# Performance work log

Hardware: AMD Instinct MI355X
Metric: run time of the kernel (lower is better)

## Reference

```python
import jax, jax.numpy as jnp
import numpy as np
from jax import lax

EPS = 1e-7
MAX_NORM = 1.0 - 1e-5

# ---- Poincare ball (c=1) primitives ----

def _norm(x):
    return jnp.sqrt(jnp.sum(x * x, -1, keepdims=True) + EPS)

def proj(x):
    n = _norm(x)
    return x * jnp.minimum(1.0, MAX_NORM / n)

def expmap0(v):
    n = _norm(v)
    return jnp.tanh(n) * v / n

def logmap0(x):
    n = _norm(x)
    return jnp.arctanh(jnp.clip(n, 0.0, MAX_NORM)) * x / n

def mobius_add(u, v):
    uv = jnp.sum(u * v, -1, keepdims=True)
    uu = jnp.sum(u * u, -1, keepdims=True)
    vv = jnp.sum(v * v, -1, keepdims=True)
    num = (1.0 + 2.0 * uv + vv) * u + (1.0 - uu) * v
    den = 1.0 + 2.0 * uv + uu * vv
    return num / den

# Mobius matvec M (x) x = expmap0(logmap0(x) @ M^T)

def gru_step(h, x, Wr, Wz, Wh, Ur, Uz, Uh, br, bz, bh):
    lh = logmap0(h)
    lx = logmap0(x)
    r = jax.nn.sigmoid(logmap0(mobius_add(mobius_add(expmap0(lh @ Wr.T), expmap0(lx @ Ur.T)), br)))
    z = jax.nn.sigmoid(logmap0(mobius_add(mobius_add(expmap0(lh @ Wz.T), expmap0(lx @ Uz.T)), bz)))
    htil = mobius_add(mobius_add(expmap0((r * lh) @ Wh.T), expmap0(lx @ Uh.T)), bh)
    delta = mobius_add(-h, htil)
    return proj(mobius_add(h, expmap0(z * logmap0(delta))))


def hyperplane_logits(X, P, A):
    # Hyperbolic MLR (Ganea et al.) without materializing [N,V,d]:
    # (-p)(+)x = (-alpha*p + beta*x) / gamma
    xx = jnp.sum(X * X, -1)                  # [N]
    pp = jnp.sum(P * P, -1)                  # [V]
    aa = jnp.sqrt(jnp.sum(A * A, -1) + EPS)  # [V]
    pa = jnp.sum(P * A, -1)                  # [V]
    px = X @ P.T                             # [N,V]
    xa = X @ A.T                             # [N,V]
    alpha = 1.0 - 2.0 * px + xx[:, None]
    beta = (1.0 - pp)[None, :]
    gamma = 1.0 - 2.0 * px + pp[None, :] * xx[:, None]
    da = (-alpha * pa[None, :] + beta * xa) / gamma
    dd = (alpha * alpha * pp[None, :] - 2.0 * alpha * beta * px + beta * beta * xx[:, None]) / (gamma * gamma)
    lam = 2.0 / (1.0 - pp)                   # conformal factor at p_k
    arg = 2.0 * da / ((1.0 - dd) * aa[None, :] + EPS)
    return (lam * aa)[None, :] * jnp.arcsinh(arg)


VOCAB, EMB, HID, LAYERS = 10000, 512, 512, 3
B, S = 16, 128


def setup_inputs() -> dict:
    key = jax.random.key(0)
    ks = jax.random.split(key, 16)
    inp = jax.random.randint(ks[0], (B, S), 0, VOCAB)
    tgt = jax.random.randint(ks[1], (B, S), 0, VOCAB)
    E = proj(0.01 * jax.random.normal(ks[2], (VOCAB, EMB), jnp.float32))
    E = E.at[0].set(0.0)  # padding_idx=0
    mk = lambda k: 0.05 * jax.random.normal(k, (LAYERS, HID, HID), jnp.float32)
    Wr, Wz, Wh = mk(ks[3]), mk(ks[4]), mk(ks[5])
    Ur, Uz, Uh = mk(ks[6]), mk(ks[7]), mk(ks[8])
    mb = lambda k: proj(0.01 * jax.random.normal(k, (LAYERS, HID), jnp.float32))
    br, bz, bh = mb(ks[9]), mb(ks[10]), mb(ks[11])
    P = proj(0.01 * jax.random.normal(ks[12], (VOCAB, HID), jnp.float32))
    A = 0.05 * jax.random.normal(ks[13], (VOCAB, HID), jnp.float32)
    return {"input": inp, "target": tgt, "E": E, "Wr": Wr, "Wz": Wz, "Wh": Wh,
            "Ur": Ur, "Uz": Uz, "Uh": Uh, "br": br, "bz": bz, "bh": bh, "P": P, "A": A}


def reference(input, target, E, Wr, Wz, Wh, Ur, Uz, Uh, br, bz, bh, P, A):
    b, s = input.shape
    x = E[input]                       # [B,S,H] points on the ball
    x = jnp.transpose(x, (1, 0, 2))    # [S,B,H]
    for l in range(LAYERS):
        params = (Wr[l], Wz[l], Wh[l], Ur[l], Uz[l], Uh[l],
                  br[l][None, :], bz[l][None, :], bh[l][None, :])
        def step(h, xt, params=params):
            h = gru_step(h, xt, *params)
            return h, h
        h0 = jnp.zeros((b, HID), x.dtype)
        _, x = lax.scan(step, h0, x)   # [S,B,H]
    X = x.transpose(1, 0, 2).reshape(-1, HID)          # [B*S,H]
    logits = hyperplane_logits(X, P, A)                # [B*S,V]
    logp = jax.nn.log_softmax(logits, axis=-1)
    nll = -jnp.take_along_axis(logp, target.reshape(-1, 1), axis=1)[:, 0]
    return jnp.mean(nll).reshape(1)
```

## Files before the change

### kernel.cpp

```cpp
#include <hip/hip_runtime.h>
#include <hip/hip_bf16.h>
#include <math.h>

#define EPSF 1e-7f
#define MAXNRM 0.99999f

static constexpr int Bb = 16, Ss = 128, Hh = 512, Vv = 10000, Ll = 3;
static constexpr int Nn = Bb * Ss;
static constexpr int VT = 625;

typedef __attribute__((ext_vector_type(4))) float f32x4;
typedef __attribute__((ext_vector_type(8))) short short8v;
typedef _Float16 h2 __attribute__((ext_vector_type(2)));

__device__ inline float4 ld4(const float* p){ return *(const float4*)p; }
__device__ inline void st4(float* p, float4 v){ *(float4*)p = v; }
__device__ inline float dot4(float4 a, float4 b){ return a.x*b.x + a.y*b.y + a.z*b.z + a.w*b.w; }
__device__ inline float sigm(float x){ return 1.f/(1.f + expf(-x)); }
__device__ inline unsigned short f2bf(float f){
  __hip_bfloat16 h = __float2bfloat16(f);
  return __builtin_bit_cast(unsigned short, h);
}
__device__ inline unsigned short f2h(float f){
  _Float16 h = (_Float16)f;
  return __builtin_bit_cast(unsigned short, h);
}
__device__ inline float rsum64f(float v){
  v+=__shfl_xor(v,32); v+=__shfl_xor(v,16); v+=__shfl_xor(v,8);
  v+=__shfl_xor(v,4);  v+=__shfl_xor(v,2);  v+=__shfl_xor(v,1); return v;
}
__device__ inline float dot4_e5m2(uint u, h2 L0, h2 L1, float acc){
  uint p01 = __builtin_amdgcn_perm(u, 0u, 0x05000400u);
  uint p23 = __builtin_amdgcn_perm(u, 0u, 0x07000600u);
  acc = __builtin_amdgcn_fdot2(__builtin_bit_cast(h2,p01), L0, acc, false);
  acc = __builtin_amdgcn_fdot2(__builtin_bit_cast(h2,p23), L1, acc, false);
  return acc;
}
__device__ inline void stg_scu(uint* p, uint v){
  asm volatile("global_store_dword %0, %1, off sc0 sc1" :: "v"(p), "v"(v) : "memory");
}
__device__ inline uint ldg_scu(const uint* p){
  uint r;
  asm volatile("global_load_dword %0, %1, off sc0 sc1\n\ts_waitcnt vmcnt(0)"
               : "=v"(r) : "v"(p) : "memory");
  return r;
}

template<int NR>
__device__ __forceinline__ void stream_e5m2_rows(const uint* __restrict__ W8m,
    const uint* src2, float (*part)[Hh], int row0, int lane, int prow){
  const int j8 = lane*8;
  const uint* W = W8m + (size_t)row0*Hh + j8;
  float acc[8] = {0,0,0,0,0,0,0,0};
  #pragma unroll 4
  for(int i=0;i<NR;i++){
    uint4 wa = *(const uint4*)(W + (size_t)i*Hh);
    uint4 wb = *(const uint4*)(W + (size_t)i*Hh + 4);
    uint2 L = *(const uint2*)&src2[(row0+i)*2];
    h2 L0=__builtin_bit_cast(h2,L.x), L1=__builtin_bit_cast(h2,L.y);
    acc[0]=dot4_e5m2(wa.x,L0,L1,acc[0]); acc[1]=dot4_e5m2(wa.y,L0,L1,acc[1]);
    acc[2]=dot4_e5m2(wa.z,L0,L1,acc[2]); acc[3]=dot4_e5m2(wa.w,L0,L1,acc[3]);
    acc[4]=dot4_e5m2(wb.x,L0,L1,acc[4]); acc[5]=dot4_e5m2(wb.y,L0,L1,acc[5]);
    acc[6]=dot4_e5m2(wb.z,L0,L1,acc[6]); acc[7]=dot4_e5m2(wb.w,L0,L1,acc[7]);
  }
  float* d = &part[prow][j8];
  *(f32x4*)d = (f32x4){acc[0],acc[1],acc[2],acc[3]};
  *(f32x4*)(d+4) = (f32x4){acc[4],acc[5],acc[6],acc[7]};
}
__device__ __forceinline__ void stream_e5m2_pair(const uint* __restrict__ WA,
    const uint* __restrict__ WB, const uint* src2, float (*part)[Hh], int tid, int j8){
  int hf = tid >> 9;
  int kq = (tid >> 6) & 7;
  const uint* W = (hf ? WB : WA) + (size_t)(kq*16)*Hh + j8;
  float acc[8] = {0,0,0,0,0,0,0,0};
  #pragma unroll 4
  for(int i=0;i<16;i++){
    uint4 wa = *(const uint4*)(W + (size_t)i*Hh);
    uint4 wb = *(const uint4*)(W + (size_t)i*Hh + 4);
    uint2 L = *(const uint2*)&src2[(kq*16+i)*2];
    h2 L0=__builtin_bit_cast(h2,L.x), L1=__builtin_bit_cast(h2,L.y);
    acc[0]=dot4_e5m2(wa.x,L0,L1,acc[0]); acc[1]=dot4_e5m2(wa.y,L0,L1,acc[1]);
    acc[2]=dot4_e5m2(wa.z,L0,L1,acc[2]); acc[3]=dot4_e5m2(wa.w,L0,L1,acc[3]);
    acc[4]=dot4_e5m2(wb.x,L0,L1,acc[4]); acc[5]=dot4_e5m2(wb.y,L0,L1,acc[5]);
    acc[6]=dot4_e5m2(wb.z,L0,L1,acc[6]); acc[7]=dot4_e5m2(wb.w,L0,L1,acc[7]);
  }
  float* d = &part[hf*8+kq][j8];
  *(f32x4*)d = (f32x4){acc[0],acc[1],acc[2],acc[3]};
  *(f32x4*)(d+4) = (f32x4){acc[4],acc[5],acc[6],acc[7]};
}

__global__ __launch_bounds__(256) void k_packW8(const float* __restrict__ Wr,
    const float* __restrict__ Wz, uint* __restrict__ W8){
  int jt = blockIdx.x, kt = blockIdx.y, lm = blockIdx.z;
  int l = lm>>1, m = lm&1;
  const float* src = (m==0?Wr:Wz) + (size_t)l*Hh*Hh;
  uint* dst = W8 + (size_t)lm*(128*Hh);
  __shared__ float t[64][65];
  int tid = threadIdx.x;
  #pragma unroll
  for(int p=0;p<4;p++){
    int row = p*16 + (tid>>4);
    int c4 = (tid&15)*4;
    st4(&t[row][c4], ld4(src + ((size_t)(jt*64+row))*Hh + kt*64 + c4));
  }
  __syncthreads();
  #pragma unroll
  for(int p=0;p<4;p++){
    int k4l = p*4 + (tid>>6);
    int j_l = tid & 63;
    uint u = 0;
    #pragma unroll
    for(int i=0;i<4;i++){
      ushort b16 = __builtin_bit_cast(ushort, (_Float16)t[j_l][k4l*4+i]);
      uint b8 = (uint)((ushort)(b16 + 0x80) >> 8);
      u |= b8 << (8*i);
    }
    dst[(size_t)(kt*16 + k4l)*Hh + jt*64 + j_l] = u;
  }
}
__global__ __launch_bounds__(256) void k_packW8s(const float* __restrict__ W, uint* __restrict__ W8){
  int jt = blockIdx.x, kt = blockIdx.y, l = blockIdx.z;
  const float* src = W + (size_t)l*Hh*Hh;
  uint* dst = W8 + (size_t)l*(128*Hh);
  __shared__ float t[64][65];
  int tid = threadIdx.x;
  #pragma unroll
  for(int p=0;p<4;p++){
    int row = p*16 + (tid>>4);
    int c4 = (tid&15)*4;
    st4(&t[row][c4], ld4(src + ((size_t)(jt*64+row))*Hh + kt*64 + c4));
  }
  __syncthreads();
  #pragma unroll
  for(int p=0;p<4;p++){
    int k4l = p*4 + (tid>>6);
    int j_l = tid & 63;
    uint u = 0;
    #pragma unroll
    for(int i=0;i<4;i++){
      ushort b16 = __builtin_bit_cast(ushort, (_Float16)t[j_l][k4l*4+i]);
      uint b8 = (uint)((ushort)(b16 + 0x80) >> 8);
      u |= b8 << (8*i);
    }
    dst[(size_t)(kt*16 + k4l)*Hh + jt*64 + j_l] = u;
  }
}

__global__ void k_predots(const float* __restrict__ XR, const float* __restrict__ XZ,
                          const float* __restrict__ XH,
                          const float* __restrict__ br, const float* __restrict__ bz,
                          const float* __restrict__ bh, float* __restrict__ pubX){
  int n = blockIdx.x; int tid = threadIdx.x;
  float s0=0,s1=0,s2=0,s3=0,s4=0,s5=0;
  for(int i=tid;i<Hh;i+=128){
    float xr=XR[(size_t)n*Hh+i], xz=XZ[(size_t)n*Hh+i], xh=XH[(size_t)n*Hh+i];
    s0+=xr*xr; s1+=xr*br[i]; s2+=xz*xz; s3+=xz*bz[i]; s4+=xh*xh; s5+=xh*bh[i];
  }
  __shared__ float red[2][6];
  s0=rsum64f(s0); s1=rsum64f(s1); s2=rsum64f(s2);
  s3=rsum64f(s3); s4=rsum64f(s4); s5=rsum64f(s5);
  int w = tid>>6;
  if((tid&63)==0){ red[w][0]=s0; red[w][1]=s1; red[w][2]=s2; red[w][3]=s3; red[w][4]=s4; red[w][5]=s5; }
  __syncthreads();
  if(tid==0){
    #pragma unroll
    for(int d=0;d<6;d++) pubX[(size_t)n*6+d] = red[0][d]+red[1][d];
  }
}

__global__ void k_pav(const float* __restrict__ P, const float* __restrict__ A,
                      float* __restrict__ pp, float* __restrict__ aa, float* __restrict__ pa){
  int w = threadIdx.x >> 6, lane = threadIdx.x & 63;
  int v = blockIdx.x*4 + w;
  const float4* Pr = (const float4*)(P + (size_t)v*Hh);
  const float4* Ar = (const float4*)(A + (size_t)v*Hh);
  float sp=0, sa=0, spa=0;
  #pragma unroll
  for(int i=0;i<2;i++){
    int k4 = lane*2 + i;
    float4 pv = Pr[k4], av = Ar[k4];
    sp += dot4(pv,pv); sa += dot4(av,av); spa += dot4(pv,av);
  }
  for(int o=32;o;o>>=1){ sp+=__shfl_down(sp,o); sa+=__shfl_down(sa,o); spa+=__shfl_down(spa,o); }
  if(lane==0){ pp[v]=sp; aa[v]=sqrtf(sa+EPSF); pa[v]=spa; }
}

__global__ void k_embed(const int* __restrict__ inp, const float* __restrict__ E, float* __restrict__ X){
  int n = blockIdx.x; int t = n >> 4, b = n & 15;
  int tok = inp[b*Ss + t];
  int i = threadIdx.x;
  st4(X + (size_t)n*Hh + i*4, ld4(E + (size_t)tok*Hh + i*4));
}

__global__ void k_logmap(const float* __restrict__ X, float* __restrict__ LX){
  int n = blockIdx.x; int t = threadIdx.x;
  __shared__ float sred[2];
  float4 v = ld4(X + (size_t)n*Hh + t*4);
  float ss = dot4(v,v);
  for(int o=32;o;o>>=1) ss += __shfl_down(ss,o);
  if((t&63)==0) sred[t>>6] = ss;
  __syncthreads();
  ss = sred[0]+sred[1];
  float nn = sqrtf(ss + EPSF);
  float sc = atanhf(fminf(nn, MAXNRM)) / nn;
  v.x*=sc; v.y*=sc; v.z*=sc; v.w*=sc;
  st4(LX + (size_t)n*Hh + t*4, v);
}

__global__ void k_expmap(float* __restrict__ XR, float* __restrict__ XZ, float* __restrict__ XH){
  float* Xp = blockIdx.y==0 ? XR : (blockIdx.y==1 ? XZ : XH);
  int n = blockIdx.x; int t = threadIdx.x;
  __shared__ float sred[2];
  float4 v = ld4(Xp + (size_t)n*Hh + t*4);
  float ss = dot4(v,v);
  for(int o=32;o;o>>=1) ss += __shfl_down(ss,o);
  if((t&63)==0) sred[t>>6] = ss;
  __syncthreads();
  ss = sred[0]+sred[1];
  float nn = sqrtf(ss + EPSF);
  float sc = tanhf(nn) / nn;
  v.x*=sc; v.y*=sc; v.z*=sc; v.w*=sc;
  st4(Xp + (size_t)n*Hh + t*4, v);
}

__global__ __launch_bounds__(256) void k_gemm(const float* __restrict__ A4,
    const float* __restrict__ U0, const float* __restrict__ U1, const float* __restrict__ U2,
    float* __restrict__ O0, float* __restrict__ O1, float* __restrict__ O2){
  __shared__ float As[16][65], Bs[16][65];
  int jb = blockIdx.x;
  int nb = blockIdx.y;
  int mat = jb >> 3; int j0 = (jb & 7)*64;
  const float* Bm = mat==0?U0 : (mat==1?U1:U2);
  float* Om       = mat==0?O0 : (mat==1?O1:O2);
  int tid = threadIdx.x;
  int lr = tid >> 2, lq = tid & 3;
  int tx = tid & 15, ty = tid >> 4;
  float acc[4][4] = {};
  for(int kb=0; kb<Hh; kb+=16){
    float4 av = ld4(A4 + (size_t)(nb*64+lr)*Hh + kb + lq*4);
    float4 bv = ld4(Bm + (size_t)(j0+lr)*Hh + kb + lq*4);
    As[lq*4+0][lr]=av.x; As[lq*4+1][lr]=av.y; As[lq*4+2][lr]=av.z; As[lq*4+3][lr]=av.w;
    Bs[lq*4+0][lr]=bv.x; Bs[lq*4+1][lr]=bv.y; Bs[lq*4+2][lr]=bv.z; Bs[lq*4+3][lr]=bv.w;
    __syncthreads();
    #pragma unroll
    for(int kk=0;kk<16;kk++){
      float a0=As[kk][ty*4+0], a1=As[kk][ty*4+1], a2=As[kk][ty*4+2], a3=As[kk][ty*4+3];
      float b0=Bs[kk][tx*4+0], b1=Bs[kk][tx*4+1], b2=Bs[kk][tx*4+2], b3=Bs[kk][tx*4+3];
      acc[0][0]+=a0*b0; acc[0][1]+=a0*b1; acc[0][2]+=a0*b2; acc[0][3]+=a0*b3;
      acc[1][0]+=a1*b0; acc[1][1]+=a1*b1; acc[1][2]+=a1*b2; acc[1][3]+=a1*b3;
      acc[2][0]+=a2*b0; acc[2][1]+=a2*b1; acc[2][2]+=a2*b2; acc[2][3]+=a2*b3;
      acc[3][0]+=a3*b0; acc[3][1]+=a3*b1; acc[3][2]+=a3*b2; acc[3][3]+=a3*b3;
    }
    __syncthreads();
  }
  for(int i=0;i<4;i++)
    for(int j2=0;j2<4;j2++)
      Om[(size_t)(nb*64+ty*4+i)*Hh + j0 + tx*4 + j2] = acc[i][j2];
}

__global__ __launch_bounds__(1024) void k_mega(
    const float* __restrict__ XR, const float* __restrict__ XZ, const float* __restrict__ XH,
    const float* __restrict__ pubX,
    const uint* __restrict__ W8, const uint* __restrict__ W8h,
    const uint* __restrict__ U8, const uint* __restrict__ U8h,
    const float* __restrict__ brA, const float* __restrict__ bzA, const float* __restrict__ bhA,
    uint* __restrict__ LH0, uint* __restrict__ LH1,
    int* __restrict__ flags0, int* __restrict__ flags1,
    float* __restrict__ Xfin){
  const int xcd = blockIdx.x & 7;
  const int layer = xcd >> 1;
  if(layer >= 3) return;
  const int b = (xcd & 1)*8 + (blockIdx.x >> 3);
  const int tid = threadIdx.x;
  const int lane = tid & 63, wv = tid >> 6;
  const int j8 = lane * 8;

  const uint* W8r = W8 + (size_t)(layer*2+0)*128*Hh;
  const uint* W8z = W8 + (size_t)(layer*2+1)*128*Hh;
  const uint* Wh8 = W8h + (size_t)layer*128*Hh;
  const uint* U8r = U8 + (size_t)(layer*2+0)*128*Hh;
  const uint* U8z = U8 + (size_t)(layer*2+1)*128*Hh;
  const uint* Uh8 = U8h + (size_t)layer*128*Hh;
  const float* br = brA + layer*Hh;
  const float* bz = bzA + layer*Hh;
  const float* bh = bhA + layer*Hh;
  uint* outLH = (layer==0)? LH0 : (layer==1)? LH1 : nullptr;
  int* outF = (layer==0)? flags0 : (layer==1)? flags1 : nullptr;
  const uint* inLH = (layer==1)? LH0 : LH1;
  int* inF = (layer==1)? flags0 : flags1;

  __shared__ float part[16][Hh];
  __shared__ float mr_s[Hh], mz_s[Hh], mur_s[Hh], muz_s[Hh];
  __shared__ uint  lh2_s[256], ap2_s[256], lx2_s[256];
  __shared__ float bias0[Hh], bias1[Hh], bias2[Hh];
  __shared__ float partA[8][16];
  __shared__ float partB[8][18];
  __shared__ float coefA_s[12], coefB_s[8], bb_s[4];

  if(tid<256) lh2_s[tid]=0u;
  for(int i=tid;i<Hh;i+=1024){ bias0[i]=br[i]; bias1[i]=bz[i]; bias2[i]=bh[i]; }
  __syncthreads();
  {
    float p0=0,p1=0,p2=0;
    if(tid<Hh){ float a=bias0[tid],b2=bias1[tid],c2=bias2[tid]; p0=a*a; p1=b2*b2; p2=c2*c2; }
    p0=rsum64f(p0); p1=rsum64f(p1); p2=rsum64f(p2);
    if(tid<Hh && lane==0){ partB[wv][0]=p0; partB[wv][1]=p1; partB[wv][2]=p2; }
    __syncthreads();
    if(tid==0){
      float a=0,b2=0,c2=0;
      for(int i=0;i<8;i++){ a+=partB[i][0]; b2+=partB[i][1]; c2+=partB[i][2]; }
      bb_s[0]=a; bb_s[1]=b2; bb_s[2]=c2;
    }
    __syncthreads();
  }

  float h = 0.f;
  float Sh = 0.f, hxh = 0.f, hbh = 0.f;

  for(int ts=0; ts<Ss; ts++){
    const size_t row = (size_t)(ts*Bb + b)*Hh;
    const size_t lrow = (size_t)(ts*Bb + b)*256;

    if(layer == 0){
      float xr=0,xz=0,xh=0;
      if(tid<512){ xr=XR[row+tid]; xz=XZ[row+tid]; xh=XH[row+tid]; }
      stream_e5m2_pair(W8r, W8z, lh2_s, part, tid, j8);
      __syncthreads();
      float mr=0.f, mz=0.f;
      if(tid<512){
        float s0=0, s1=0;
        #pragma unroll
        for(int q=0;q<8;q++){ s0+=part[q][tid]; s1+=part[8+q][tid]; }
        mr=s0; mz=s1; mr_s[tid]=s0;
        float brc=bias0[tid], bzc=bias1[tid], bhc=bias2[tid];
        float p0=mr*mr, p1=mr*xr, p2=mr*brc, p3=mz*mz, p4=mz*xz, p5=mz*bzc, p6=h*xh, p7=h*bhc;
        p0=rsum64f(p0); p1=rsum64f(p1); p2=rsum64f(p2); p3=rsum64f(p3);
        p4=rsum64f(p4); p5=rsum64f(p5); p6=rsum64f(p6); p7=rsum64f(p7);
        if(lane==0){
          partA[wv][0]=p0; partA[wv][1]=p1; partA[wv][2]=p2; partA[wv][3]=p3;
          partA[wv][4]=p4; partA[wv][5]=p5; partA[wv][6]=p6; partA[wv][7]=p7;
        }
      }
      __syncthreads();
      if(tid==0){
        float s[8];
        #pragma unroll
        for(int d=0;d<8;d++){
          float x=0;
          for(int i=0;i<8;i++) x+=partA[i][d];
          s[d]=x;
        }
        hxh=s[6]; hbh=s[7];
        const float* px = pubX + (size_t)(ts*Bb+b)*6;
        float xrxr=px[0], xrbr=px[1], xzxz=px[2], xzbz=px[3];
        float bbr=bb_s[0], bbz=bb_s[1];
        float nm=sqrtf(s[0]+EPSF), se=tanhf(nm)/nm;
        float uv=se*s[1], uu=se*se*s[0];
        float den=1.f+2.f*uv+uu*xrxr;
        float a1=(1.f+2.f*uv+xrxr)*se/den, a2=(1.f-uu)/den;
        float uv2=a1*s[2]+a2*xrbr;
        float uu2=a1*a1*s[0]+2.f*a1*a2*s[1]+a2*a2*xrxr;
        float den2=1.f+2.f*uv2+uu2*bbr;
        float b1=(1.f+2.f*uv2+bbr)/den2, b2c=(1.f-uu2)/den2;
        float c1=b1*a1, c2=b1*a2, c3=b2c;
        float n2sq=c1*c1*s[0]+c2*c2*xrxr+c3*c3*bbr+2.f*(c1*c2*s[1]+c1*c3*s[2]+c2*c3*xrbr);
        float nn2=sqrtf(n2sq+EPSF);
        float s_r=atanhf(fminf(nn2,MAXNRM))/nn2;
        coefA_s[0]=s_r*c1; coefA_s[1]=s_r*c2; coefA_s[2]=s_r*c3;
        float nmz=sqrtf(s[3]+EPSF), sez=tanhf(nmz)/nmz;
        float uvz=sez*s[4], uuz=sez*sez*s[3];
        float denz=1.f+2.f*uvz+uuz*xzxz;
        float az1=(1.f+2.f*uvz+xzxz)*sez/denz, az2=(1.f-uuz)/denz;
        float uvz2=az1*s[5]+az2*xzbz;
        float uuz2=az1*az1*s[3]+2.f*az1*az2*s[4]+az2*az2*xzxz;
        float denz2=1.f+2.f*uvz2+uuz2*bbz;
        float bz1=(1.f+2.f*uvz2+bbz)/denz2, bz2=(1.f-uuz2)/denz2;
        float cz1=bz1*az1, cz2=bz1*az2, cz3=bz2;
        float nz2sq=cz1*cz1*s[3]+cz2*cz2*xzxz+cz3*cz3*bbz+2.f*(cz1*cz2*s[4]+cz1*cz3*s[5]+cz2*cz3*xzbz);
        float nnz2=sqrtf(nz2sq+EPSF);
        float s_z=atanhf(fminf(nnz2,MAXNRM))/nnz2;
        coefA_s[3]=s_z*cz1; coefA_s[4]=s_z*cz2; coefA_s[5]=s_z*cz3;
        coefA_s[6]=px[4]; coefA_s[7]=px[4]; coefA_s[8]=px[5];
      }
      __syncthreads();
      if(tid<256){
        int e0 = tid*2;
        float ca=coefA_s[0], cb=coefA_s[1], cc2=coefA_s[2];
        h2 lp = __builtin_bit_cast(h2, lh2_s[tid]);
        float r0 = sigm(ca*mr_s[e0]   + cb*XR[row+e0]   + cc2*bias0[e0]);
        float r1 = sigm(ca*mr_s[e0+1] + cb*XR[row+e0+1] + cc2*bias0[e0+1]);
        ap2_s[tid] = (uint)f2h(r0*(float)lp[0]) | ((uint)f2h(r1*(float)lp[1])<<16);
      }
      __syncthreads();
      stream_e5m2_rows<8>(Wh8, ap2_s, part, (tid>>6)*8, lane, tid>>6);
      __syncthreads();
      float mh=0.f, z=0.f;
      if(tid<512){
        float s=0;
        #pragma unroll
        for(int q=0;q<16;q++) s+=part[q][tid];
        mh=s;
        float bhc=bias2[tid], bzc=bias1[tid];
        z = sigm(coefA_s[3]*mz + coefA_s[4]*xz + coefA_s[5]*bzc);
        float eh=z*h, em=z*mh, ex=z*xh, eb=z*bhc;
        float p[18] = {mh*mh, mh*xh, mh*bhc, h*mh,
                       eh*eh, eh*em, eh*ex, eh*eb,
                       em*em, em*ex, em*eb, ex*ex, ex*eb, eb*eb,
                       h*eh, h*em, h*ex, h*eb};
        #pragma unroll
        for(int d=0;d<18;d++) p[d]=rsum64f(p[d]);
        if(lane==0){
          #pragma unroll
          for(int d=0;d<18;d++) partB[wv][d]=p[d];
        }
      }
      __syncthreads();
      if(tid==0){
        float dsum[18];
        #pragma unroll
        for(int d=0;d<18;d++){
          float x=0;
          for(int i=0;i<8;i++) x+=partB[i][d];
          dsum[d]=x;
        }
        float d0=dsum[0], d1=dsum[1], d2=dsum[2], d3=dsum[3];
        float Ghh=dsum[4], Ghm=dsum[5], Ghx=dsum[6], Ghb=dsum[7];
        float Gmm=dsum[8], Gmx=dsum[9], Gmb=dsum[10];
        float Gxx=dsum[11], Gxb=dsum[12], Gbb=dsum[13];
        float Heh=dsum[14], Hem=dsum[15], Hex=dsum[16], Heb=dsum[17];
        float xhxh=coefA_s[7], xhbh=coefA_s[8];
        float bbh=bb_s[2]; float Shb=Sh;
        float nm3=sqrtf(d0+EPSF), se3=tanhf(nm3)/nm3;
        float uvh=se3*d1, uuh=se3*se3*d0;
        float denh=1.f+2.f*uvh+uuh*xhxh;
        float a1p=(1.f+2.f*uvh+xhxh)*se3/denh, a2p=(1.f-uuh)/denh;
        float uv2h=a1p*d2+a2p*xhbh;
        float uu2h=a1p*a1p*d0+2.f*a1p*a2p*d1+a2p*a2p*xhxh;
        float den2h=1.f+2.f*uv2h+uu2h*bbh;
        float b1p=(1.f+2.f*uv2h+bbh)/den2h, b2p=(1.f-uu2h)/den2h;
        float c1p=b1p*a1p, c2p=b1p*a2p, c3p=b2p;
        float h_htil=c1p*d3+c2p*hxh+c3p*hbh;
        float htil2=c1p*c1p*d0+c2p*c2p*xhxh+c3p*c3p*bbh
                  +2.f*(c1p*c2p*d1+c1p*c3p*d2+c2p*c3p*xhbh);
        float denD=1.f-2.f*h_htil+Shb*htil2;
        float dd1=(1.f-2.f*h_htil+htil2)/denD, dd2=(1.f-Shb)/denD;
        float g0=-dd1, g1=dd2*c1p, g2=dd2*c2p, g3=dd2*c3p;
        float del2=g0*g0*Shb+g1*g1*d0+g2*g2*xhxh+g3*g3*bbh
                 +2.f*(g0*g1*d3+g0*g2*hxh+g0*g3*hbh+g1*g2*d1+g1*g3*d2+g2*g3*xhbh);
        float ndl=sqrtf(del2+EPSF);
        float sld=atanhf(fminf(ndl,MAXNRM))/ndl;
        float Qe=g0*g0*Ghh+g1*g1*Gmm+g2*g2*Gxx+g3*g3*Gbb
               +2.f*(g0*g1*Ghm+g0*g2*Ghx+g0*g3*Ghb+g1*g2*Gmx+g1*g3*Gmb+g2*g3*Gxb);
        float Le=g0*Heh+g1*Hem+g2*Hex+g3*Heb;
        float Sww=sld*sld*Qe;
        float Shw=sld*Le;
        float nw=sqrtf(Sww+EPSF), sew=tanhf(nw)/nw;
        float uvw=sew*Shw, vvw=sew*sew*Sww;
        float denw=1.f+2.f*uvw+Shb*vvw;
        float q1=(1.f+2.f*uvw+vvw)/denw, q2=((1.f-Shb)/denw)*sew;
        float n2h=q1*q1*Shb+2.f*q1*q2*Shw+q2*q2*Sww;
        float nrm=sqrtf(n2h+EPSF);
        float scl=fminf(1.f, MAXNRM/nrm);
        float Shn=scl*scl*n2h;
        float nh2=sqrtf(Shn+EPSF);
        float slh=atanhf(fminf(nh2,MAXNRM))/nh2;
        coefB_s[0]=scl*q1; coefB_s[1]=scl*q2*sld;
        coefB_s[2]=g0; coefB_s[3]=g1; coefB_s[4]=g2; coefB_s[5]=g3;
        coefB_s[6]=slh;
        Sh=Shn;
      }
      __syncthreads();
      if(tid<512){
        float qc1=coefB_s[0], qc2=coefB_s[1];
        float g0=coefB_s[2], g1=coefB_s[3], g2=coefB_s[4], g3=coefB_s[5];
        float slh=coefB_s[6];
        float dl = g0*h + g1*mh + g2*xh + g3*bias2[tid];
        float hn = qc1*h + qc2*z*dl;
        h = hn;
        float lh = slh*hn;
        float lhp = __shfl_xor(lh, 1);
        if(!(tid&1)){
          uint pk = (uint)f2h(lh) | ((uint)f2h(lhp)<<16);
          lh2_s[tid>>1] = pk;
          stg_scu(outLH + lrow + (tid>>1), pk);
        }
      }
      __syncthreads();
      if(tid==0) __hip_atomic_store(outF + b*Ss + ts, 1, __ATOMIC_RELAXED, __HIP_MEMORY_SCOPE_AGENT);
    } else {
      if(tid < 512){
        if(wv < 4) stream_e5m2_rows<32>(W8r, lh2_s, part, wv*32, lane, wv);
        else       stream_e5m2_rows<32>(W8z, lh2_s, part, (wv-4)*32, lane, wv);
      } else if(tid < 768){
        int idx = tid - 512;
        while(__hip_atomic_load(inF + b*Ss + ts, __ATOMIC_RELAXED, __HIP_MEMORY_SCOPE_AGENT) == 0)
          __builtin_amdgcn_s_sleep(1);
        lx2_s[idx] = ldg_scu(inLH + lrow + idx);
      }
      __syncthreads();

      float mr=0.f, mz=0.f;
      if(tid < 512){
        mr = part[0][tid]+part[1][tid]+part[2][tid]+part[3][tid];
        mz = part[4][tid]+part[5][tid]+part[6][tid]+part[7][tid];
        mr_s[tid]=mr; mz_s[tid]=mz;
        float p0=mr*mr, p1=mr*bias0[tid], p2=mz*mz, p3=mz*bias1[tid];
        p0=rsum64f(p0); p1=rsum64f(p1); p2=rsum64f(p2); p3=rsum64f(p3);
        if(lane==0){ partA[wv][0]=p0; partA[wv][1]=p1; partA[wv][2]=p2; partA[wv][3]=p3; }
      } else {
        if(wv < 12) stream_e5m2_rows<32>(U8r, lx2_s, part, (wv-8)*32, lane, wv);
        else        stream_e5m2_rows<32>(U8z, lx2_s, part, (wv-12)*32, lane, wv);
      }
      __syncthreads();

      if(tid < 512){
        stream_e5m2_rows<16>(Uh8, lx2_s, part, wv*16, lane, wv);
      } else {
        int j = tid - 512;
        float mur = part[8][j]+part[9][j]+part[10][j]+part[11][j];
        float muz = part[12][j]+part[13][j]+part[14][j]+part[15][j];
        mur_s[j]=mur; muz_s[j]=muz;
        float p5=mur*mur, p6=mur*bias0[j], p7=muz*muz, p8=muz*bias1[j];
        float p9=mr_s[j]*mur, p10=mz_s[j]*muz;
        p5=rsum64f(p5); p6=rsum64f(p6); p7=rsum64f(p7);
        p8=rsum64f(p8); p9=rsum64f(p9); p10=rsum64f(p10);
        if(lane==0){
          partA[wv-8][5]=p5; partA[wv-8][6]=p6; partA[wv-8][7]=p7;
          partA[wv-8][8]=p8; partA[wv-8][9]=p9; partA[wv-8][10]=p10;
        }
      }
      __syncthreads();

      float muh=0.f;
      if(tid<512){
        float s=0;
        #pragma unroll
        for(int q=0;q<8;q++) s+=part[q][tid];
        muh=s;
        float bhc=bias2[tid];
        float p11=muh*muh, p12=h*muh, p13=muh*bhc, p14=h*bhc;
        p11=rsum64f(p11); p12=rsum64f(p12); p13=rsum64f(p13); p14=rsum64f(p14);
        if(lane==0){ partA[wv][11]=p11; partA[wv][12]=p12; partA[wv][13]=p13; partA[wv][14]=p14; }
      }
      __syncthreads();

      if(tid==0){
        float S[15];
        #pragma unroll
        for(int d=0;d<15;d++){
          float xS=0;
          for(int i=0;i<8;i++) xS+=partA[i][d];
          S[d]=xS;
        }
        float bbr=bb_s[0], bbz=bb_s[1];
        float nur=sqrtf(S[5]+EPSF), se_r=tanhf(nur)/nur;
        float nuz=sqrtf(S[7]+EPSF), se_z=tanhf(nuz)/nuz;
        float nuh=sqrtf(S[11]+EPSF), se_h=tanhf(nuh)/nuh;
        float s0=S[0], s1=se_r*S[9], s2=S[1];
        float xrxr=se_r*se_r*S[5], xrbr=se_r*S[6];
        float s3=S[2], s4=se_z*S[10], s5=S[3];
        float xzxz=se_z*se_z*S[7], xzbz=se_z*S[8];
        hxh = se_h*S[12]; hbh = S[14];
        float xhxh=se_h*se_h*S[11], xhbh=se_h*S[13];
        float nm=sqrtf(s0+EPSF), se=tanhf(nm)/nm;
        float uv=se*s1, uu=se*se*s0;
        float den=1.f+2.f*uv+uu*xrxr;
        float a1=(1.f+2.f*uv+xrxr)*se/den, a2=(1.f-uu)/den;
        float uv2=a1*s2+a2*xrbr;
        float uu2=a1*a1*s0+2.f*a1*a2*s1+a2*a2*xrxr;
        float den2=1.f+2.f*uv2+uu2*bbr;
        float b1=(1.f+2.f*uv2+bbr)/den2, b2c=(1.f-uu2)/den2;
        float c1=b1*a1, c2=b1*a2, c3=b2c;
        float n2sq=c1*c1*s0+c2*c2*xrxr+c3*c3*bbr+2.f*(c1*c2*s1+c1*c3*s2+c2*c3*xrbr);
        float nn2=sqrtf(n2sq+EPSF);
        float s_r=atanhf(fminf(nn2,MAXNRM))/nn2;
        coefA_s[0]=s_r*c1; coefA_s[1]=s_r*c2*se_r; coefA_s[2]=s_r*c3;
        float nmz=sqrtf(s3+EPSF), sez=tanhf(nmz)/nmz;
        float uvz=sez*s4, uuz=sez*sez*s3;
        float denz=1.f+2.f*uvz+uuz*xzxz;
        float az1=(1.f+2.f*uvz+xzxz)*sez/denz, az2=(1.f-uuz)/denz;
        float uvz2=az1*s5+az2*xzbz;
        float uuz2=az1*az1*s3+2.f*az1*az2*s4+az2*az2*xzxz;
        float denz2=1.f+2.f*uvz2+uuz2*bbz;
        float bz1=(1.f+2.f*uvz2+bbz)/denz2, bz2=(1.f-uuz2)/denz2;
        float cz1=bz1*az1, cz2=bz1*az2, cz3=bz2;
        float nz2sq=cz1*cz1*s3+cz2*cz2*xzxz+cz3*cz3*bbz+2.f*(cz1*cz2*s4+cz1*cz3*s5+cz2*cz3*xzbz);
        float nnz2=sqrtf(nz2sq+EPSF);
        float s_z=atanhf(fminf(nnz2,MAXNRM))/nnz2;
        coefA_s[3]=s_z*cz1; coefA_s[4]=s_z*cz2*se_z; coefA_s[5]=s_z*cz3;
        coefA_s[6]=se_h; coefA_s[7]=xhxh; coefA_s[8]=xhbh;
      }
      __syncthreads();

      if(tid<256){
        int e0 = tid*2;
        float ca=coefA_s[0], cbp=coefA_s[1], cc2=coefA_s[2];
        h2 lp = __builtin_bit_cast(h2, lh2_s[tid]);
        float r0 = sigm(ca*mr_s[e0]   + cbp*mur_s[e0]   + cc2*bias0[e0]);
        float r1 = sigm(ca*mr_s[e0+1] + cbp*mur_s[e0+1] + cc2*bias0[e0+1]);
        ap2_s[tid] = (uint)f2h(r0*(float)lp[0]) | ((uint)f2h(r1*(float)lp[1])<<16);
      }
      __syncthreads();

      stream_e5m2_rows<8>(Wh8, ap2_s, part, (tid>>6)*8, lane, tid>>6);
      __syncthreads();

      float mh=0.f, z=0.f;
      if(tid<512){
        float s=0;
        #pragma unroll
        for(int q=0;q<16;q++) s+=part[q][tid];
        mh=s;
        float se_h = coefA_s[6];
        float xh = se_h*muh;
        float bhc=bias2[tid], bzc=bias1[tid];
        z = sigm(coefA_s[3]*mz + coefA_s[4]*muz_s[tid] + coefA_s[5]*bzc);
        float eh=z*h, em=z*mh, ex=z*xh, eb=z*bhc;
        float p[18] = {mh*mh, mh*xh, mh*bhc, h*mh,
                       eh*eh, eh*em, eh*ex, eh*eb,
                       em*em, em*ex, em*eb, ex*ex, ex*eb, eb*eb,
                       h*eh, h*em, h*ex, h*eb};
        #pragma unroll
        for(int d=0;d<18;d++) p[d]=rsum64f(p[d]);
        if(lane==0){
          #pragma unroll
          for(int d=0;d<18;d++) partB[wv][d]=p[d];
        }
      }
      __syncthreads();

      if(tid==0){
        float dsum[18];
        #pragma unroll
        for(int d=0;d<18;d++){
          float xS=0;
          for(int i=0;i<8;i++) xS+=partB[i][d];
          dsum[d]=xS;
        }
        float d0=dsum[0], d1=dsum[1], d2=dsum[2], d3=dsum[3];
        float Ghh=dsum[4], Ghm=dsum[5], Ghx=dsum[6], Ghb=dsum[7];
        float Gmm=dsum[8], Gmx=dsum[9], Gmb=dsum[10];
        float Gxx=dsum[11], Gxb=dsum[12], Gbb=dsum[13];
        float Heh=dsum[14], Hem=dsum[15], Hex=dsum[16], Heb=dsum[17];
        float xhxh=coefA_s[7], xhbh=coefA_s[8];
        float bbh=bb_s[2]; float Shb=Sh;
        float nm3=sqrtf(d0+EPSF), se3=tanhf(nm3)/nm3;
        float uvh=se3*d1, uuh=se3*se3*d0;
        float denh=1.f+2.f*uvh+uuh*xhxh;
        float a1p=(1.f+2.f*uvh+xhxh)*se3/denh, a2p=(1.f-uuh)/denh;
        float uv2h=a1p*d2+a2p*xhbh;
        float uu2h=a1p*a1p*d0+2.f*a1p*a2p*d1+a2p*a2p*xhxh;
        float den2h=1.f+2.f*uv2h+uu2h*bbh;
        float b1p=(1.f+2.f*uv2h+bbh)/den2h, b2p=(1.f-uu2h)/den2h;
        float c1p=b1p*a1p, c2p=b1p*a2p, c3p=b2p;
        float h_htil=c1p*d3+c2p*hxh+c3p*hbh;
        float htil2=c1p*c1p*d0+c2p*c2p*xhxh+c3p*c3p*bbh
                  +2.f*(c1p*c2p*d1+c1p*c3p*d2+c2p*c3p*xhbh);
        float denD=1.f-2.f*h_htil+Shb*htil2;
        float dd1=(1.f-2.f*h_htil+htil2)/denD, dd2=(1.f-Shb)/denD;
        float g0=-dd1, g1=dd2*c1p, g2=dd2*c2p, g3=dd2*c3p;
        float del2=g0*g0*Shb+g1*g1*d0+g2*g2*xhxh+g3*g3*bbh
                 +2.f*(g0*g1*d3+g0*g2*hxh+g0*g3*hbh+g1*g2*d1+g1*g3*d2+g2*g3*xhbh);
        float ndl=sqrtf(del2+EPSF);
        float sld=atanhf(fminf(ndl,MAXNRM))/ndl;
        float Qe=g0*g0*Ghh+g1*g1*Gmm+g2*g2*Gxx+g3*g3*Gbb
               +2.f*(g0*g1*Ghm+g0*g2*Ghx+g0*g3*Ghb+g1*g2*Gmx+g1*g3*Gmb+g2*g3*Gxb);
        float Le=g0*Heh+g1*Hem+g2*Hex+g3*Heb;
        float Sww=sld*sld*Qe;
        float Shw=sld*Le;
        float nw=sqrtf(Sww+EPSF), sew=tanhf(nw)/nw;
        float uvw=sew*Shw, vvw=sew*sew*Sww;
        float denw=1.f+2.f*uvw+Shb*vvw;
        float q1=(1.f+2.f*uvw+vvw)/denw, q2=((1.f-Shb)/denw)*sew;
        float n2h=q1*q1*Shb+2.f*q1*q2*Shw+q2*q2*Sww;
        float nrm=sqrtf(n2h+EPSF);
        float scl=fminf(1.f, MAXNRM/nrm);
        float Shn=scl*scl*n2h;
        float nh2=sqrtf(Shn+EPSF);
        float slh=atanhf(fminf(nh2,MAXNRM))/nh2;
        coefB_s[0]=scl*q1; coefB_s[1]=scl*q2*sld;
        coefB_s[2]=g0; coefB_s[3]=g1; coefB_s[4]=g2; coefB_s[5]=g3;
        coefB_s[6]=slh;
        Sh=Shn;
      }
      __syncthreads();

      if(tid<512){
        float qc1=coefB_s[0], qc2=coefB_s[1];
        float g0=coefB_s[2], g1=coefB_s[3], g2=coefB_s[4], g3=coefB_s[5];
        float slh=coefB_s[6];
        float xh = coefA_s[6]*muh;
        float dl = g0*h + g1*mh + g2*xh + g3*bias2[tid];
        float hn = qc1*h + qc2*z*dl;
        h = hn;
        if(layer==2) Xfin[row + tid] = hn;
        float lh = slh*hn;
        float lhp = __shfl_xor(lh, 1);
        if(!(tid&1)){
          uint pk = (uint)f2h(lh) | ((uint)f2h(lhp)<<16);
          lh2_s[tid>>1] = pk;
          if(layer==1) stg_scu(outLH + lrow + (tid>>1), pk);
        }
      }
      __syncthreads();
      if(layer==1 && tid==0)
        __hip_atomic_store(outF + b*Ss + ts, 1, __ATOMIC_RELAXED, __HIP_MEMORY_SCOPE_AGENT);
    }
  }
}

__global__ __launch_bounds__(256) void k_packF(const float* __restrict__ src, ushort* __restrict__ dst){
  int vt = blockIdx.x;
  __shared__ float rows[16][516];
  int tid = threadIdx.x;
  #pragma unroll
  for(int p=0;p<8;p++){
    int idx = p*256 + tid;
    int row = idx >> 7, c4 = idx & 127;
    st4(&rows[row][c4*4], ld4(src + ((size_t)vt*16+row)*Hh + c4*4));
  }
  __syncthreads();
  #pragma unroll
  for(int p=0;p<4;p++){
    int idx = p*256 + tid;
    int kt = idx >> 6, lane = idx & 63;
    int vloc = lane & 15, k0 = kt*32 + ((lane>>4)&3)*8;
    union { ushort u[8]; uint4 v; } tt;
    #pragma unroll
    for(int i=0;i<8;i++) tt.u[i] = f2bf(rows[vloc][k0+i]);
    *(uint4*)(dst + (((size_t)vt*16 + kt)*64 + lane)*8) = tt.v;
  }
}

__global__ __launch_bounds__(256) void k_mlr2(
    const ushort* __restrict__ Xf, const ushort* __restrict__ Pf, const ushort* __restrict__ Af,
    const float* __restrict__ X, const float* __restrict__ pp, const float* __restrict__ aa,
    const float* __restrict__ pa, const int* __restrict__ tgt,
    float* __restrict__ pm, float* __restrict__ tl){
  int rb = blockIdx.x;
  int sp = blockIdx.y;
  int tid = threadIdx.x, lane = tid&63, w = tid>>6;
  __shared__ ushort Axf[4*16*64*8];
  __shared__ float xxp[64][4];
  __shared__ float xxs[64];
  #pragma unroll
  for(int p=0;p<16;p++){
    int idx = p*256 + tid;
    ((uint4*)Axf)[idx] = ((const uint4*)Xf)[(size_t)rb*4096 + idx];
  }
  {
    int row = tid>>2, seg = tid&3;
    const float* xr = X + ((size_t)rb*64 + row)*Hh + seg*128;
    float s=0;
    #pragma unroll
    for(int i=0;i<32;i++){ float4 v4 = ld4(xr+i*4); s += dot4(v4,v4); }
    xxp[row][seg]=s;
  }
  __syncthreads();
  if(tid<64) xxs[tid] = xxp[tid][0]+xxp[tid][1]+xxp[tid][2]+xxp[tid][3];
  __syncthreads();

  float mM[16], sS[16]; int tokv[16];
  #pragma unroll
  for(int rt=0;rt<4;rt++)
    #pragma unroll
    for(int i=0;i<4;i++){
      int idx=rt*4+i;
      int rr = rb*64 + rt*16 + (lane>>4)*4 + i;
      tokv[idx] = tgt[(rr&15)*Ss + (rr>>4)];
      mM[idx] = -3.0e38f; sS[idx]=0.f;
    }

  for(int vt = sp*4 + w; vt < VT; vt += 32){
    int v = vt*16 + (lane&15);
    float ppv = pp[v], aav = aa[v], pav = pa[v];
    f32x4 aP[4], aA[4];
    #pragma unroll
    for(int rt=0;rt<4;rt++){ aP[rt]=(f32x4){0,0,0,0}; aA[rt]=(f32x4){0,0,0,0}; }
    const short8v* Pb = (const short8v*)(Pf + (size_t)vt*8192);
    const short8v* Ab = (const short8v*)(Af + (size_t)vt*8192);
    #pragma unroll
    for(int kt=0;kt<16;kt++){
      short8v bP = Pb[kt*64+lane];
      short8v bA = Ab[kt*64+lane];
      #pragma unroll
      for(int rt=0;rt<4;rt++){
        short8v a = *(const short8v*)&Axf[(((size_t)rt*16+kt)*64+lane)*8];
        aP[rt] = __builtin_amdgcn_mfma_f32_16x16x32_bf16(a, bP, aP[rt], 0,0,0);
        aA[rt] = __builtin_amdgcn_mfma_f32_16x16x32_bf16(a, bA, aA[rt], 0,0,0);
      }
    }
    float be = 1.f - ppv;
    float lamaa = (2.f/be)*aav;
    #pragma unroll
    for(int rt=0;rt<4;rt++)
      #pragma unroll
      for(int i=0;i<4;i++){
        int idx = rt*4+i;
        int rl = rt*16 + (lane>>4)*4 + i;
        float px = aP[rt][i], xa = aA[rt][i];
        float xx = xxs[rl];
        float al = 1.f - 2.f*px + xx;
        float gm = 1.f - 2.f*px + ppv*xx;
        float da = (-al*pav + be*xa)/gm;
        float dd = (al*al*ppv - 2.f*al*be*px + be*be*xx)/(gm*gm);
        float arg = 2.f*da/((1.f-dd)*aav + EPSF);
        float lg = lamaa*asinhf(arg);
        if(v == tokv[idx]) tl[rb*64 + rl] = lg;
        if(lg > mM[idx]){ sS[idx] = sS[idx]*expf(mM[idx]-lg) + 1.f; mM[idx]=lg; }
        else sS[idx] += expf(lg - mM[idx]);
      }
  }
  #pragma unroll
  for(int o=1;o<16;o<<=1){
    #pragma unroll
    for(int idx=0;idx<16;idx++){
      float m2 = __shfl_xor(mM[idx], o);
      float s2 = __shfl_xor(sS[idx], o);
      float M = fmaxf(mM[idx], m2);
      sS[idx] = sS[idx]*expf(mM[idx]-M) + s2*expf(m2-M);
      mM[idx] = M;
    }
  }
  if((lane&15)==0){
    #pragma unroll
    for(int rt=0;rt<4;rt++)
      #pragma unroll
      for(int i=0;i<4;i++){
        int idx=rt*4+i;
        int rr = rb*64 + rt*16 + (lane>>4)*4 + i;
        pm[((size_t)rr*32 + sp*4 + w)*2+0] = mM[idx];
        pm[((size_t)rr*32 + sp*4 + w)*2+1] = sS[idx];
      }
  }
}

__global__ void k_final(const float* __restrict__ pm, const float* __restrict__ tl, float* __restrict__ out){
  int tid = threadIdx.x;
  __shared__ float sred[4];
  float acc = 0.f;
  for(int q=0;q<8;q++){
    int rr = q*256 + tid;
    float M = -3.0e38f;
    for(int s=0;s<32;s++) M = fmaxf(M, pm[((size_t)rr*32+s)*2]);
    float Ssum = 0.f;
    for(int s=0;s<32;s++) Ssum += pm[((size_t)rr*32+s)*2+1]*expf(pm[((size_t)rr*32+s)*2]-M);
    acc += (M + logf(Ssum)) - tl[rr];
  }
  for(int o=32;o;o>>=1) acc += __shfl_down(acc,o);
  if((tid&63)==0) sred[tid>>6] = acc;
  __syncthreads();
  if(tid==0) out[0] = (sred[0]+sred[1]+sred[2]+sred[3]) / 2048.f;
}

extern "C" void kernel_launch(void* const* d_in, const int* in_sizes, int n_in,
                              void* d_out, int out_size, void* d_ws, size_t ws_size,
                              hipStream_t stream){
  const int* inp = (const int*)d_in[0];
  const int* tgt = (const int*)d_in[1];
  const float* E  = (const float*)d_in[2];
  const float* Wr = (const float*)d_in[3];
  const float* Wz = (const float*)d_in[4];
  const float* Wh = (const float*)d_in[5];
  const float* Ur = (const float*)d_in[6];
  const float* Uz = (const float*)d_in[7];
  const float* Uh = (const float*)d_in[8];
  const float* br = (const float*)d_in[9];
  const float* bz = (const float*)d_in[10];
  const float* bh = (const float*)d_in[11];
  const float* P  = (const float*)d_in[12];
  const float* A  = (const float*)d_in[13];
  float* out = (float*)d_out;
  float* w = (float*)d_ws;
  size_t o = 0;
  auto take = [&](size_t n){ float* p = w + o; o += n; return p; };
  float* Xa  = take((size_t)Nn*Hh);
  float* Xb  = take((size_t)Nn*Hh);
  float* LX  = take((size_t)Nn*Hh);
  float* XR  = take((size_t)Nn*Hh);
  float* XZ  = take((size_t)Nn*Hh);
  float* XH  = take((size_t)Nn*Hh);
  uint*  LH0 = (uint*)take((size_t)Nn*256);
  uint*  LH1 = (uint*)take((size_t)Nn*256);
  uint*  W8h = (uint*)take((size_t)3*128*Hh);
  uint*  W8  = (uint*)take((size_t)6*128*Hh);
  uint*  U8h = (uint*)take((size_t)3*128*Hh);
  uint*  U8  = (uint*)take((size_t)6*128*Hh);
  float* pubX = take((size_t)Nn*6);
  float* pp  = take(10240);
  float* aa  = take(10240);
  float* pa  = take(10240);
  float* pm  = take((size_t)Nn*32*2);
  float* tl  = take((size_t)Nn);
  int* flags = (int*)take(2*(size_t)Bb*Ss);
  if(ws_size < o*sizeof(float)) return;
  int* flags0 = flags;
  int* flags1 = flags + Bb*Ss;

  hipLaunchKernelGGL(k_packW8s, dim3(8,8,3), dim3(256), 0, stream, Wh, W8h);
  hipLaunchKernelGGL(k_packW8s, dim3(8,8,3), dim3(256), 0, stream, Uh, U8h);
  hipLaunchKernelGGL(k_packW8, dim3(8,8,6), dim3(256), 0, stream, Wr, Wz, W8);
  hipLaunchKernelGGL(k_packW8, dim3(8,8,6), dim3(256), 0, stream, Ur, Uz, U8);
  hipLaunchKernelGGL(k_pav, dim3(2500), dim3(256), 0, stream, P,A, pp,aa,pa);
  hipLaunchKernelGGL(k_embed, dim3(Nn), dim3(128), 0, stream, inp, E, Xa);
  hipLaunchKernelGGL(k_logmap, dim3(Nn), dim3(128), 0, stream, Xa, LX);
  hipLaunchKernelGGL(k_gemm, dim3(24,32), dim3(256), 0, stream, LX,
                     Ur, Uz, Uh, XR, XZ, XH);
  hipLaunchKernelGGL(k_expmap, dim3(Nn,3), dim3(128), 0, stream, XR,XZ,XH);
  hipLaunchKernelGGL(k_predots, dim3(Nn), dim3(128), 0, stream, XR,XZ,XH, br, bz, bh, pubX);
  hipMemsetAsync(flags, 0, 2*(size_t)Bb*Ss*sizeof(int), stream);
  hipLaunchKernelGGL(k_mega, dim3(64), dim3(1024), 0, stream,
                     XR,XZ,XH, pubX, W8,W8h,U8,U8h, br,bz,bh,
                     LH0, LH1, flags0, flags1, Xb);
  ushort* Pf = (ushort*)LX;
  ushort* Af = Pf + (size_t)VT*16*64*8;
  ushort* Xf = (ushort*)Xa;
  hipLaunchKernelGGL(k_packF, dim3(VT), dim3(256), 0, stream, P, Pf);
  hipLaunchKernelGGL(k_packF, dim3(VT), dim3(256), 0, stream, A, Af);
  hipLaunchKernelGGL(k_packF, dim3(128), dim3(256), 0, stream, Xb, Xf);
  hipLaunchKernelGGL(k_mlr2, dim3(32,8), dim3(256), 0, stream, Xf, Pf, Af, Xb,
                     pp, aa, pa, tgt, pm, tl);
  hipLaunchKernelGGL(k_final, dim3(1), dim3(256), 0, stream, pm, tl, out);
}
```

Before: 3.969 ms.

## Overlap U-gate streams with W streams and split Uh into separate buffer

In the layer>0 recurrent step, the upper 8 waves no longer only wait for the previous layer's flag and load lx. Each wave now loads its own slice of lx and streams the Ur/Uz rows itself, running alongside the Wr/Wz streams in the same phase. The Uh stream is moved into a new partC buffer so it can overlap with the mr/mz/mur/muz reductions, and one barrier phase is dropped. The cost is extra shared memory for partC. Each wave syncs only on its own lx slice, which relies on intra-wave ordering of the LDS write before the read.

```diff
diff --git a/kernel.cpp b/kernel.cpp
--- a/kernel.cpp
+++ b/kernel.cpp
@@ -46,9 +46,9 @@
   return r;
 }
 
-template<int NR>
+template<int NR, int PR>
 __device__ __forceinline__ void stream_e5m2_rows(const uint* __restrict__ W8m,
-    const uint* src2, float (*part)[Hh], int row0, int lane, int prow){
+    const uint* src2, float (*dst)[Hh], int row0, int lane, int prow){
   const int j8 = lane*8;
   const uint* W = W8m + (size_t)row0*Hh + j8;
   float acc[8] = {0,0,0,0,0,0,0,0};
@@ -63,7 +63,7 @@
     acc[4]=dot4_e5m2(wb.x,L0,L1,acc[4]); acc[5]=dot4_e5m2(wb.y,L0,L1,acc[5]);
     acc[6]=dot4_e5m2(wb.z,L0,L1,acc[6]); acc[7]=dot4_e5m2(wb.w,L0,L1,acc[7]);
   }
-  float* d = &part[prow][j8];
+  float* d = &dst[prow][j8];
   *(f32x4*)d = (f32x4){acc[0],acc[1],acc[2],acc[3]};
   *(f32x4*)(d+4) = (f32x4){acc[4],acc[5],acc[6],acc[7]};
 }
@@ -290,7 +290,8 @@
   int* inF = (layer==1)? flags0 : flags1;
 
   __shared__ float part[16][Hh];
-  __shared__ float mr_s[Hh], mz_s[Hh], mur_s[Hh], muz_s[Hh];
+  __shared__ float partC[8][Hh];
+  __shared__ float mr_s[Hh], mur_s[Hh];
   __shared__ uint  lh2_s[256], ap2_s[256], lx2_s[256];
   __shared__ float bias0[Hh], bias1[Hh], bias2[Hh];
   __shared__ float partA[8][16];
@@ -392,7 +393,7 @@
         ap2_s[tid] = (uint)f2h(r0*(float)lp[0]) | ((uint)f2h(r1*(float)lp[1])<<16);
       }
       __syncthreads();
-      stream_e5m2_rows<8>(Wh8, ap2_s, part, (tid>>6)*8, lane, tid>>6);
+      stream_e5m2_rows<8,16>(Wh8, ap2_s, part, (tid>>6)*8, lane, tid>>6);
       __syncthreads();
       float mh=0.f, z=0.f;
       if(tid<512){
@@ -489,45 +490,41 @@
       if(tid==0) __hip_atomic_store(outF + b*Ss + ts, 1, __ATOMIC_RELAXED, __HIP_MEMORY_SCOPE_AGENT);
     } else {
       if(tid < 512){
-        if(wv < 4) stream_e5m2_rows<32>(W8r, lh2_s, part, wv*32, lane, wv);
-        else       stream_e5m2_rows<32>(W8z, lh2_s, part, (wv-4)*32, lane, wv);
-      } else if(tid < 768){
-        int idx = tid - 512;
-        while(__hip_atomic_load(inF + b*Ss + ts, __ATOMIC_RELAXED, __HIP_MEMORY_SCOPE_AGENT) == 0)
-          __builtin_amdgcn_s_sleep(1);
-        lx2_s[idx] = ldg_scu(inLH + lrow + idx);
-      }
-      __syncthreads();
-
-      float mr=0.f, mz=0.f;
+        if(wv < 4) stream_e5m2_rows<32,16>(W8r, lh2_s, part, wv*32, lane, wv);
+        else       stream_e5m2_rows<32,16>(W8z, lh2_s, part, (wv-4)*32, lane, wv);
+      } else {
+        int uw = wv - 8;
+        int rbase = (uw & 3) * 32;
+        if(lane==0){
+          while(__hip_atomic_load(inF + b*Ss + ts, __ATOMIC_RELAXED, __HIP_MEMORY_SCOPE_AGENT) == 0)
+            __builtin_amdgcn_s_sleep(1);
+        }
+        lx2_s[rbase*2 + lane] = ldg_scu(inLH + lrow + rbase*2 + lane);
+        if(uw < 4) stream_e5m2_rows<32,16>(U8r, lx2_s, part, rbase, lane, wv);
+        else       stream_e5m2_rows<32,16>(U8z, lx2_s, part, rbase, lane, wv);
+      }
+      __syncthreads();
+
+      float mr=0.f, mz=0.f, mur=0.f, muz=0.f;
       if(tid < 512){
-        mr = part[0][tid]+part[1][tid]+part[2][tid]+part[3][tid];
-        mz = part[4][tid]+part[5][tid]+part[6][tid]+part[7][tid];
-        mr_s[tid]=mr; mz_s[tid]=mz;
-        float p0=mr*mr, p1=mr*bias0[tid], p2=mz*mz, p3=mz*bias1[tid];
+        mr  = part[0][tid]+part[1][tid]+part[2][tid]+part[3][tid];
+        mz  = part[4][tid]+part[5][tid]+part[6][tid]+part[7][tid];
+        mur = part[8][tid]+part[9][tid]+part[10][tid]+part[11][tid];
+        muz = part[12][tid]+part[13][tid]+part[14][tid]+part[15][tid];
+        mr_s[tid]=mr; mur_s[tid]=mur;
+        float brc=bias0[tid], bzc=bias1[tid];
+        float p0=mr*mr, p1=mr*brc, p2=mz*mz, p3=mz*bzc;
+        float p5=mur*mur, p6=mur*brc, p7=muz*muz, p8=muz*bzc, p9=mr*mur, p10=mz*muz;
         p0=rsum64f(p0); p1=rsum64f(p1); p2=rsum64f(p2); p3=rsum64f(p3);
-        if(lane==0){ partA[wv][0]=p0; partA[wv][1]=p1; partA[wv][2]=p2; partA[wv][3]=p3; }
-      } else {
-        if(wv < 12) stream_e5m2_rows<32>(U8r, lx2_s, part, (wv-8)*32, lane, wv);
-        else        stream_e5m2_rows<32>(U8z, lx2_s, part, (wv-12)*32, lane, wv);
-      }
-      __syncthreads();
-
-      if(tid < 512){
-        stream_e5m2_rows<16>(Uh8, lx2_s, part, wv*16, lane, wv);
-      } else {
-        int j = tid - 512;
-        float mur = part[8][j]+part[9][j]+part[10][j]+part[11][j];
-        float muz = part[12][j]+part[13][j]+part[14][j]+part[15][j];
-        mur_s[j]=mur; muz_s[j]=muz;
-        float p5=mur*mur, p6=mur*bias0[j], p7=muz*muz, p8=muz*bias1[j];
-        float p9=mr_s[j]*mur, p10=mz_s[j]*muz;
         p5=rsum64f(p5); p6=rsum64f(p6); p7=rsum64f(p7);
         p8=rsum64f(p8); p9=rsum64f(p9); p10=rsum64f(p10);
         if(lane==0){
-          partA[wv-8][5]=p5; partA[wv-8][6]=p6; partA[wv-8][7]=p7;
-          partA[wv-8][8]=p8; partA[wv-8][9]=p9; partA[wv-8][10]=p10;
-        }
+          partA[wv][0]=p0; partA[wv][1]=p1; partA[wv][2]=p2; partA[wv][3]=p3;
+          partA[wv][5]=p5; partA[wv][6]=p6; partA[wv][7]=p7;
+          partA[wv][8]=p8; partA[wv][9]=p9; partA[wv][10]=p10;
+        }
+      } else {
+        stream_e5m2_rows<16,8>(Uh8, lx2_s, partC, (wv-8)*16, lane, wv-8);
       }
       __syncthreads();
 
@@ -535,7 +532,7 @@
       if(tid<512){
         float s=0;
         #pragma unroll
-        for(int q=0;q<8;q++) s+=part[q][tid];
+        for(int q=0;q<8;q++) s+=partC[q][tid];
         muh=s;
         float bhc=bias2[tid];
         float p11=muh*muh, p12=h*muh, p13=muh*bhc, p14=h*bhc;
@@ -602,7 +599,7 @@
       }
       __syncthreads();
 
-      stream_e5m2_rows<8>(Wh8, ap2_s, part, (tid>>6)*8, lane, tid>>6);
+      stream_e5m2_rows<8,16>(Wh8, ap2_s, part, (tid>>6)*8, lane, tid>>6);
       __syncthreads();
 
       float mh=0.f, z=0.f;
@@ -614,7 +611,7 @@
         float se_h = coefA_s[6];
         float xh = se_h*muh;
         float bhc=bias2[tid], bzc=bias1[tid];
-        z = sigm(coefA_s[3]*mz + coefA_s[4]*muz_s[tid] + coefA_s[5]*bzc);
+        z = sigm(coefA_s[3]*mz + coefA_s[4]*muz + coefA_s[5]*bzc);
         float eh=z*h, em=z*mh, ex=z*xh, eb=z*bhc;
         float p[18] = {mh*mh, mh*xh, mh*bhc, h*mh,
                        eh*eh, eh*em, eh*ex, eh*eb,
```

Result: no change. 4.003 ms (+0.9%).
